# Kernel tuning notes

Measured on AMD Instinct MI355X. Metric: run time of the kernel, lower is better.

## Reference

```python
import jax, jax.numpy as jnp
import numpy as np

B, N, C = 4, 4096, 1024
NUM_HEADS = 16
HEAD_DIM = C // NUM_HEADS


def setup_inputs() -> dict:
    key = jax.random.key(0)
    k1, k2, k3, k4 = jax.random.split(key, 4)
    s_in = 1.0 / np.sqrt(C)
    return {
        "x": jax.random.normal(k1, (B, N, C), dtype=jnp.float32),
        "H": 64,
        "W": 64,
        "Wqkv": jax.random.normal(k2, (3 * C, C), dtype=jnp.float32) * s_in,
        "Wproj": jax.random.normal(k3, (C, C), dtype=jnp.float32) * s_in,
        "bproj": jnp.zeros((C,), dtype=jnp.float32),
        "alpha": jnp.ones((NUM_HEADS,), dtype=jnp.float32),
    }


def reference(x, H, W, Wqkv, Wproj, bproj, alpha):
    Bb, Nn, Cc = x.shape
    h, d = NUM_HEADS, HEAD_DIM
    # qkv: [B, N, 3C] -> [3, B, h, N, d]
    qkv = jnp.einsum('bnc,oc->bno', x, Wqkv)
    qkv = qkv.reshape(Bb, Nn, 3, h, d).transpose(2, 0, 3, 1, 4)
    q, k, v = qkv[0], qkv[1], qkv[2]  # each [B, h, N, d]
    # channel attention: contract over tokens N -> [B, h, d, d]
    attn = jnp.einsum('bhnd,bhne->bhde', k, q) / alpha[None, :, None, None]
    attn = jax.nn.softmax(attn, axis=-1)
    # (dropout is identity in eval/reference mode)
    # head_out: [B, h, d, N] -> transpose -> [B, N, h, d] -> concat heads
    out = jnp.einsum('bhde,bhne->bhdn', attn, v)
    out = out.transpose(0, 3, 1, 2).reshape(Bb, Nn, Cc)
    return jnp.einsum('bnc,oc->bno', out, Wproj) + bproj
```

## Files before the change

### kernel.cpp

```cpp
#include <hip/hip_runtime.h>
#include <hip/hip_bf16.h>
#include <cstdint>
#include <cstddef>

typedef unsigned short u16;
typedef __bf16 bf16x8 __attribute__((ext_vector_type(8)));
typedef float f32x4 __attribute__((ext_vector_type(4)));
typedef unsigned short u16x4 __attribute__((ext_vector_type(4)));
typedef unsigned short u16x8 __attribute__((ext_vector_type(8)));

#define AS1(p) ((__attribute__((address_space(1))) void*)(p))
#define AS3(p) ((__attribute__((address_space(3))) void*)(p))

__device__ __forceinline__ float bf2f(u16 u) {
  unsigned v = ((unsigned)u) << 16; float f; __builtin_memcpy(&f, &v, 4); return f;
}
__device__ __forceinline__ u16 f2bf(float f) {
  unsigned u; __builtin_memcpy(&u, &f, 4);
  u += 0x7FFFu + ((u >> 16) & 1u);
  return (u16)(u >> 16);
}

__global__ __launch_bounds__(256) void convert_kernel(const float* __restrict__ src,
                                                      u16* __restrict__ dst, int n4) {
  int i = blockIdx.x * blockDim.x + threadIdx.x;
  int stride = gridDim.x * blockDim.x;
  for (; i < n4; i += stride) {
    float4 v = ((const float4*)src)[i];
    u16x4 o;
    o.x = f2bf(v.x); o.y = f2bf(v.y); o.z = f2bf(v.z); o.w = f2bf(v.w);
    ((u16x4*)dst)[i] = o;
  }
}

__global__ __launch_bounds__(256) void convert_split_kernel(const float* __restrict__ src,
                                                            u16* __restrict__ hi,
                                                            u16* __restrict__ lo, int n4) {
  int i = blockIdx.x * blockDim.x + threadIdx.x;
  int stride = gridDim.x * blockDim.x;
  for (; i < n4; i += stride) {
    float4 v = ((const float4*)src)[i];
    u16x4 oh, ol;
    oh.x = f2bf(v.x); ol.x = f2bf(v.x - bf2f(oh.x));
    oh.y = f2bf(v.y); ol.y = f2bf(v.y - bf2f(oh.y));
    oh.z = f2bf(v.z); ol.z = f2bf(v.z - bf2f(oh.z));
    oh.w = f2bf(v.w); ol.w = f2bf(v.w - bf2f(oh.w));
    ((u16x4*)hi)[i] = oh;
    ((u16x4*)lo)[i] = ol;
  }
}

__global__ __launch_bounds__(256) void transpose_split_kernel(const float* __restrict__ x,
                                                              u16* __restrict__ Xb,
                                                              u16* __restrict__ XThi,
                                                              u16* __restrict__ XTlo) {
  __shared__ u16 lhi[64 * 72];
  __shared__ u16 llo[64 * 72];
  const int t  = threadIdx.x;
  const int nT = blockIdx.x, cT = blockIdx.y, b = blockIdx.z;
  const size_t xbase = ((size_t)b * 4096 + nT * 64) * 1024 + cT * 64;
  const int c4 = (t & 15) * 4;
  const int r0 = t >> 4;
#pragma unroll
  for (int j = 0; j < 4; ++j) {
    int r = r0 + j * 16;
    float4 v = *(const float4*)(x + xbase + (size_t)r * 1024 + c4);
    u16x4 hi;
    hi.x = f2bf(v.x); hi.y = f2bf(v.y); hi.z = f2bf(v.z); hi.w = f2bf(v.w);
    *(u16x4*)(Xb + xbase + (size_t)r * 1024 + c4) = hi;
    u16 lo[4];
    lo[0] = f2bf(v.x - bf2f(hi.x)); lo[1] = f2bf(v.y - bf2f(hi.y));
    lo[2] = f2bf(v.z - bf2f(hi.z)); lo[3] = f2bf(v.w - bf2f(hi.w));
    u16 hia[4] = { hi.x, hi.y, hi.z, hi.w };
#pragma unroll
    for (int i = 0; i < 4; ++i) {
      lhi[(c4 + i) * 72 + r] = hia[i];
      llo[(c4 + i) * 72 + r] = lo[i];
    }
  }
  __syncthreads();
  const int c  = t >> 2;
  const int n0 = (t & 3) * 16;
  const size_t tbase = ((size_t)b * 1024 + cT * 64 + c) * 4096 + nT * 64 + n0;
  *(u16x8*)(XThi + tbase)     = *(const u16x8*)(lhi + c * 72 + n0);
  *(u16x8*)(XThi + tbase + 8) = *(const u16x8*)(lhi + c * 72 + n0 + 8);
  *(u16x8*)(XTlo + tbase)     = *(const u16x8*)(llo + c * 72 + n0);
  *(u16x8*)(XTlo + tbase + 8) = *(const u16x8*)(llo + c * 72 + n0 + 8);
}

template<bool OUT_BF16, bool HAS_BIAS>
__global__ __launch_bounds__(512, 2) void gemm_pipe(const u16* __restrict__ A,
                                                    const u16* __restrict__ B,
                                                    void* __restrict__ Cv,
                                                    const float* __restrict__ bias,
                                                    int M, int N, int K,
                                                    size_t sA, size_t sB, size_t sC) {
  __shared__ __align__(16) u16 lds[4][2][8192];
  const int tid  = threadIdx.x;
  const int lane = tid & 63;
  const int wave = tid >> 6;
  const int wm = wave >> 2, wn = wave & 3;
  const int rowTile = blockIdx.x * 256;
  const int colTile = blockIdx.y * 256;
  A += (size_t)blockIdx.z * sA;
  B += (size_t)blockIdx.z * sB;

  size_t srcA[2], srcB[2];
  int ldsOff[2];
#pragma unroll
  for (int j = 0; j < 2; ++j) {
    const int L = j * 512 + tid;
    const int sr = L >> 3;
    const int slot = (L & 7) ^ (sr & 7);
    const int r  = (sr << 1) | (slot >> 2);
    const int kq = slot & 3;
    srcA[j] = (size_t)(rowTile + r) * K + kq * 8;
    srcB[j] = (size_t)(colTile + r) * K + kq * 8;
    ldsOff[j] = (j * 512 + (tid & 448)) * 16;
  }

  const int m15 = lane & 15, kq4 = lane >> 4;
  const int r0a = wm * 128 + m15, sa0 = r0a >> 1;
  const int idxA0 = sa0 * 64 + (((((r0a & 1) << 2) | kq4)) ^ (sa0 & 7)) * 8;
  const int r0b = wn * 64 + m15, sb0 = r0b >> 1;
  const int idxB0 = sb0 * 64 + (((((r0b & 1) << 2) | kq4)) ^ (sb0 & 7)) * 8;

  const int NT = K >> 5;

  auto stageA = [&](int tt) {
    char* d = (char*)&lds[tt & 3][0][0];
    const int kt = tt << 5;
#pragma unroll
    for (int j = 0; j < 2; ++j)
      __builtin_amdgcn_global_load_lds(AS1(A + srcA[j] + kt), AS3(d + ldsOff[j]), 16, 0, 0);
  };
  auto stageB = [&](int tt) {
    char* d = (char*)&lds[tt & 3][1][0];
    const int kt = tt << 5;
#pragma unroll
    for (int j = 0; j < 2; ++j)
      __builtin_amdgcn_global_load_lds(AS1(B + srcB[j] + kt), AS3(d + ldsOff[j]), 16, 0, 0);
  };

  stageA(0); stageB(0);
  if (NT > 1) { stageA(1); stageB(1); }
  if (NT > 2) { stageA(2); stageB(2); }
  if (NT > 2) asm volatile("s_waitcnt vmcnt(8)" ::: "memory");
  else        asm volatile("s_waitcnt vmcnt(0)" ::: "memory");
  __builtin_amdgcn_sched_barrier(0);
  __builtin_amdgcn_s_barrier();
  __builtin_amdgcn_sched_barrier(0);

  f32x4 acc[8][4] = {};
  for (int t = 0; t < NT; ++t) {
    const u16* bufA = &lds[t & 3][0][0];
    const u16* bufB = &lds[t & 3][1][0];
    bf16x8 a[8], bfr[4];
#pragma unroll
    for (int ni = 0; ni < 4; ++ni) bfr[ni] = *(const bf16x8*)(bufB + idxB0 + ni * 512);
#pragma unroll
    for (int mi = 0; mi < 4; ++mi) a[mi] = *(const bf16x8*)(bufA + idxA0 + mi * 512);
    if (t + 3 < NT) stageA(t + 3);
    __builtin_amdgcn_sched_barrier(0);
    __builtin_amdgcn_s_barrier();
    __builtin_amdgcn_sched_barrier(0);
    __builtin_amdgcn_s_setprio(1);
#pragma unroll
    for (int mi = 0; mi < 4; ++mi)
#pragma unroll
      for (int ni = 0; ni < 4; ++ni)
        acc[mi][ni] = __builtin_amdgcn_mfma_f32_16x16x32_bf16(a[mi], bfr[ni], acc[mi][ni], 0, 0, 0);
    __builtin_amdgcn_s_setprio(0);
    __builtin_amdgcn_sched_barrier(0);
    __builtin_amdgcn_s_barrier();
    __builtin_amdgcn_sched_barrier(0);
#pragma unroll
    for (int mi = 4; mi < 8; ++mi) a[mi] = *(const bf16x8*)(bufA + idxA0 + mi * 512);
    if (t + 3 < NT) stageB(t + 3);
    __builtin_amdgcn_sched_barrier(0);
    __builtin_amdgcn_s_barrier();
    __builtin_amdgcn_sched_barrier(0);
    __builtin_amdgcn_s_setprio(1);
#pragma unroll
    for (int mi = 4; mi < 8; ++mi)
#pragma unroll
      for (int ni = 0; ni < 4; ++ni)
        acc[mi][ni] = __builtin_amdgcn_mfma_f32_16x16x32_bf16(a[mi], bfr[ni], acc[mi][ni], 0, 0, 0);
    __builtin_amdgcn_s_setprio(0);
    if (t < NT - 1) {
      if (t + 3 < NT)      asm volatile("s_waitcnt vmcnt(8)" ::: "memory");
      else if (t + 2 < NT) asm volatile("s_waitcnt vmcnt(4)" ::: "memory");
      else                 asm volatile("s_waitcnt vmcnt(0)" ::: "memory");
    }
    __builtin_amdgcn_sched_barrier(0);
    __builtin_amdgcn_s_barrier();
    __builtin_amdgcn_sched_barrier(0);
  }

  const int crow0 = rowTile + wm * 128 + (lane >> 4) * 4;
  const int ccol0 = colTile + wn * 64 + m15;
  if constexpr (OUT_BF16) {
    u16* C = (u16*)Cv + (size_t)blockIdx.z * sC;
#pragma unroll
    for (int mi = 0; mi < 8; ++mi)
#pragma unroll
      for (int ni = 0; ni < 4; ++ni) {
        const int col = ccol0 + ni * 16;
        const float bv = HAS_BIAS ? bias[col] : 0.f;
#pragma unroll
        for (int r = 0; r < 4; ++r)
          C[(size_t)(crow0 + mi * 16 + r) * N + col] = f2bf(acc[mi][ni][r] + bv);
      }
  } else {
    float* C = (float*)Cv + (size_t)blockIdx.z * sC;
#pragma unroll
    for (int mi = 0; mi < 8; ++mi)
#pragma unroll
      for (int ni = 0; ni < 4; ++ni) {
        const int col = ccol0 + ni * 16;
        const float bv = HAS_BIAS ? bias[col] : 0.f;
#pragma unroll
        for (int r = 0; r < 4; ++r)
          C[(size_t)(crow0 + mi * 16 + r) * N + col] = acc[mi][ni][r] + bv;
      }
  }
}

__device__ __forceinline__ void pipe4_core(const u16* __restrict__ pAh,
                                           const u16* __restrict__ pAl,
                                           const u16* __restrict__ pBh,
                                           const u16* __restrict__ pBl,
                                           u16* lds, int ldsByteOff,
                                           int idxA0, int idxB0, int NT,
                                           f32x4 acc[4][2]) {
  auto stage2A = [&](int tt) {
    u16* d = lds + (tt & 3) * 16384;
    const int kt = tt << 5;
    __builtin_amdgcn_global_load_lds(AS1(pAh + kt), AS3((char*)d + ldsByteOff), 16, 0, 0);
    __builtin_amdgcn_global_load_lds(AS1(pAl + kt), AS3((char*)(d + 4096) + ldsByteOff), 16, 0, 0);
  };
  auto stage2B = [&](int tt) {
    u16* d = lds + (tt & 3) * 16384 + 8192;
    const int kt = tt << 5;
    __builtin_amdgcn_global_load_lds(AS1(pBh + kt), AS3((char*)d + ldsByteOff), 16, 0, 0);
    __builtin_amdgcn_global_load_lds(AS1(pBl + kt), AS3((char*)(d + 4096) + ldsByteOff), 16, 0, 0);
  };

  stage2A(0); stage2B(0);
  stage2A(1); stage2B(1);
  stage2A(2); stage2B(2);
  asm volatile("s_waitcnt vmcnt(8)" ::: "memory");
  __builtin_amdgcn_sched_barrier(0);
  __builtin_amdgcn_s_barrier();
  __builtin_amdgcn_sched_barrier(0);

  for (int t = 0; t < NT; ++t) {
    const u16* base = lds + (t & 3) * 16384;
    bf16x8 ah[4], al[4], bh[2], bl[2];
    bh[0] = *(const bf16x8*)(base + 8192 + idxB0);
    bh[1] = *(const bf16x8*)(base + 8192 + idxB0 + 512);
    bl[0] = *(const bf16x8*)(base + 12288 + idxB0);
    bl[1] = *(const bf16x8*)(base + 12288 + idxB0 + 512);
    ah[0] = *(const bf16x8*)(base + idxA0);
    ah[1] = *(const bf16x8*)(base + idxA0 + 512);
    al[0] = *(const bf16x8*)(base + 4096 + idxA0);
    al[1] = *(const bf16x8*)(base + 4096 + idxA0 + 512);
    if (t + 3 < NT) stage2A(t + 3);
    __builtin_amdgcn_sched_barrier(0);
    __builtin_amdgcn_s_barrier();
    __builtin_amdgcn_sched_barrier(0);
    __builtin_amdgcn_s_setprio(1);
#pragma unroll
    for (int mi = 0; mi < 2; ++mi)
#pragma unroll
      for (int ni = 0; ni < 2; ++ni) {
        acc[mi][ni] = __builtin_amdgcn_mfma_f32_16x16x32_bf16(ah[mi], bh[ni], acc[mi][ni], 0, 0, 0);
        acc[mi][ni] = __builtin_amdgcn_mfma_f32_16x16x32_bf16(ah[mi], bl[ni], acc[mi][ni], 0, 0, 0);
        acc[mi][ni] = __builtin_amdgcn_mfma_f32_16x16x32_bf16(al[mi], bh[ni], acc[mi][ni], 0, 0, 0);
      }
    __builtin_amdgcn_s_setprio(0);
    __builtin_amdgcn_sched_barrier(0);
    __builtin_amdgcn_s_barrier();
    __builtin_amdgcn_sched_barrier(0);
    ah[2] = *(const bf16x8*)(base + idxA0 + 1024);
    ah[3] = *(const bf16x8*)(base + idxA0 + 1536);
    al[2] = *(const bf16x8*)(base + 4096 + idxA0 + 1024);
    al[3] = *(const bf16x8*)(base + 4096 + idxA0 + 1536);
    if (t + 3 < NT) stage2B(t + 3);
    __builtin_amdgcn_sched_barrier(0);
    __builtin_amdgcn_s_barrier();
    __builtin_amdgcn_sched_barrier(0);
    __builtin_amdgcn_s_setprio(1);
#pragma unroll
    for (int mi = 2; mi < 4; ++mi)
#pragma unroll
      for (int ni = 0; ni < 2; ++ni) {
        acc[mi][ni] = __builtin_amdgcn_mfma_f32_16x16x32_bf16(ah[mi], bh[ni], acc[mi][ni], 0, 0, 0);
        acc[mi][ni] = __builtin_amdgcn_mfma_f32_16x16x32_bf16(ah[mi], bl[ni], acc[mi][ni], 0, 0, 0);
        acc[mi][ni] = __builtin_amdgcn_mfma_f32_16x16x32_bf16(al[mi], bh[ni], acc[mi][ni], 0, 0, 0);
      }
    __builtin_amdgcn_s_setprio(0);
    if (t < NT - 1) {
      if (t + 3 < NT)      asm volatile("s_waitcnt vmcnt(8)" ::: "memory");
      else if (t + 2 < NT) asm volatile("s_waitcnt vmcnt(4)" ::: "memory");
      else                 asm volatile("s_waitcnt vmcnt(0)" ::: "memory");
    }
    __builtin_amdgcn_sched_barrier(0);
    __builtin_amdgcn_s_barrier();
    __builtin_amdgcn_sched_barrier(0);
  }
}

__global__ __launch_bounds__(512, 2) void gram_pipe(const u16* __restrict__ XThi,
                                                    const u16* __restrict__ XTlo,
                                                    float* __restrict__ Gpart) {
  __shared__ __align__(16) u16 lds[4 * 4 * 4096];
  const int tid = threadIdx.x, lane = tid & 63, wave = tid >> 6;
  const int wm = wave >> 2, wn = wave & 3;
  const int bid = blockIdx.x;
  int b, rT, cT, slice, k0, NT;
  if (bid < 64) {
    b = bid & 3; const int j = bid >> 2;
    rT = cT = j >> 1; slice = j & 1; k0 = slice * 2048; NT = 64;
  } else {
    const int e = bid - 64; b = e & 3;
    const int idx = e >> 2; const int tile = idx >> 2, kq = idx & 3;
    int t = tile, rt = 0;
    while (t >= 7 - rt) { t -= 7 - rt; ++rt; }
    const int ct = rt + 1 + t;
    rT = rt; cT = ct;
    if (kq >= 2) { rT = ct; cT = rt; }
    slice = kq & 1; k0 = kq * 1024; NT = 32;
  }
  const int rowTile = rT * 128, colTile = cT * 128;
  const u16* Ah = XThi + ((size_t)b << 22);
  const u16* Al = XTlo + ((size_t)b << 22);

  const int sr = tid >> 3;
  const int slot = (tid & 7) ^ (sr & 7);
  const int r = (sr << 1) | (slot >> 2);
  const int kq8 = (slot & 3) * 8;
  const u16* pAh = Ah + (size_t)(rowTile + r) * 4096 + k0 + kq8;
  const u16* pAl = Al + (size_t)(rowTile + r) * 4096 + k0 + kq8;
  const u16* pBh = Ah + (size_t)(colTile + r) * 4096 + k0 + kq8;
  const u16* pBl = Al + (size_t)(colTile + r) * 4096 + k0 + kq8;
  const int ldsByteOff = (tid & 448) * 16;

  const int m15 = lane & 15, kq4 = lane >> 4;
  const int r0a = wm * 64 + m15, sa0 = r0a >> 1;
  const int idxA0 = sa0 * 64 + (((((r0a & 1) << 2) | kq4)) ^ (sa0 & 7)) * 8;
  const int r0b = wn * 32 + m15, sb0 = r0b >> 1;
  const int idxB0 = sb0 * 64 + (((((r0b & 1) << 2) | kq4)) ^ (sb0 & 7)) * 8;

  f32x4 acc[4][2] = {};
  pipe4_core(pAh, pAl, pBh, pBl, lds, ldsByteOff, idxA0, idxB0, NT, acc);

  float* out = Gpart + ((size_t)(slice * 4 + b) << 20);
  const int crow0 = rowTile + wm * 64 + (lane >> 4) * 4;
  const int ccol0 = colTile + wn * 32 + m15;
#pragma unroll
  for (int mi = 0; mi < 4; ++mi)
#pragma unroll
    for (int ni = 0; ni < 2; ++ni)
#pragma unroll
      for (int r4 = 0; r4 < 4; ++r4)
        out[(size_t)(crow0 + mi * 16 + r4) * 1024 + ccol0 + ni * 16] = acc[mi][ni][r4];
}

__global__ __launch_bounds__(256) void gram_reduce_split(const float* __restrict__ Gp,
                                                         u16* __restrict__ Ghi,
                                                         u16* __restrict__ Glo) {
  const int rt = blockIdx.x, ct = blockIdx.y, b = blockIdx.z;
  const bool diag128 = (rt >> 1) == (ct >> 1);
  const float* s0 = Gp + ((size_t)b << 20);
  const float* s1 = Gp + ((size_t)(4 + b) << 20);
  __shared__ float lT[64 * 68];
  const int t = threadIdx.x;
  const int r = t >> 2;
  const int c16 = (t & 3) * 16;

  if (!diag128) {
    const size_t bb = (size_t)(ct * 64 + r) * 1024 + rt * 64 + c16;
#pragma unroll
    for (int q = 0; q < 4; ++q) {
      float4 v0 = *(const float4*)(s0 + bb + q * 4);
      float4 v1 = *(const float4*)(s1 + bb + q * 4);
      float4 s = { v0.x + v1.x, v0.y + v1.y, v0.z + v1.z, v0.w + v1.w };
      *(float4*)(lT + r * 68 + c16 + q * 4) = s;
    }
    __syncthreads();
  }

  const size_t ab = (size_t)(rt * 64 + r) * 1024 + ct * 64 + c16;
  const size_t ob = ((size_t)b << 20) + ab;
#pragma unroll
  for (int q = 0; q < 4; ++q) {
    float4 v0 = *(const float4*)(s0 + ab + q * 4);
    float4 v1 = *(const float4*)(s1 + ab + q * 4);
    float g[4] = { v0.x + v1.x, v0.y + v1.y, v0.z + v1.z, v0.w + v1.w };
    if (!diag128) {
#pragma unroll
      for (int i = 0; i < 4; ++i) g[i] += lT[(c16 + q * 4 + i) * 68 + r];
    }
    u16x4 oh, ol;
    oh.x = f2bf(g[0]); ol.x = f2bf(g[0] - bf2f(oh.x));
    oh.y = f2bf(g[1]); ol.y = f2bf(g[1] - bf2f(oh.y));
    oh.z = f2bf(g[2]); ol.z = f2bf(g[2] - bf2f(oh.z));
    oh.w = f2bf(g[3]); ol.w = f2bf(g[3] - bf2f(oh.w));
    *(u16x4*)(Ghi + ob + q * 4) = oh;
    *(u16x4*)(Glo + ob + q * 4) = ol;
  }
}

__global__ __launch_bounds__(512, 2) void tprime_pipe(const u16* __restrict__ Wqh,
                                                      const u16* __restrict__ Wql,
                                                      const u16* __restrict__ Ghi,
                                                      const u16* __restrict__ Glo,
                                                      u16* __restrict__ Tph,
                                                      u16* __restrict__ Tpl) {
  __shared__ __align__(16) u16 lds[4 * 4 * 4096];
  const int tid = threadIdx.x, lane = tid & 63, wave = tid >> 6;
  const int wm = wave >> 2, wn = wave & 3;
  const int bid = blockIdx.x;
  const int b = bid & 3, tile = bid >> 2;
  const int rowTile = (tile >> 3) * 128, colTile = (tile & 7) * 128;
  const size_t zoff = (size_t)b << 20;

  const int sr = tid >> 3;
  const int slot = (tid & 7) ^ (sr & 7);
  const int r = (sr << 1) | (slot >> 2);
  const int kq8 = (slot & 3) * 8;
  const u16* pAh = Wqh + (size_t)(rowTile + r) * 1024 + kq8;
  const u16* pAl = Wql + (size_t)(rowTile + r) * 1024 + kq8;
  const u16* pBh = Ghi + zoff + (size_t)(colTile + r) * 1024 + kq8;
  const u16* pBl = Glo + zoff + (size_t)(colTile + r) * 1024 + kq8;
  const int ldsByteOff = (tid & 448) * 16;

  const int m15 = lane & 15, kq4 = lane >> 4;
  const int r0a = wm * 64 + m15, sa0 = r0a >> 1;
  const int idxA0 = sa0 * 64 + (((((r0a & 1) << 2) | kq4)) ^ (sa0 & 7)) * 8;
  const int r0b = wn * 32 + m15, sb0 = r0b >> 1;
  const int idxB0 = sb0 * 64 + (((((r0b & 1) << 2) | kq4)) ^ (sb0 & 7)) * 8;

  f32x4 acc[4][2] = {};
  pipe4_core(pAh, pAl, pBh, pBl, lds, ldsByteOff, idxA0, idxB0, 32, acc);

  const int crow0 = rowTile + wm * 64 + (lane >> 4) * 4;
  const int ccol0 = colTile + wn * 32 + m15;
#pragma unroll
  for (int mi = 0; mi < 4; ++mi)
#pragma unroll
    for (int ni = 0; ni < 2; ++ni)
#pragma unroll
      for (int r4 = 0; r4 < 4; ++r4) {
        float v = acc[mi][ni][r4];
        u16 hi = f2bf(v);
        u16 lo = f2bf(v - bf2f(hi));
        size_t off = zoff + (size_t)(crow0 + mi * 16 + r4) * 1024 + ccol0 + ni * 16;
        Tph[off] = hi;
        Tpl[off] = lo;
      }
}

__global__ __launch_bounds__(256) void s_softmax_kernel(const u16* __restrict__ Wqh,
                                                        const u16* __restrict__ Wql,
                                                        const u16* __restrict__ Tph,
                                                        const u16* __restrict__ Tpl,
                                                        const float* __restrict__ alpha,
                                                        u16* __restrict__ attnT) {
  const int h = blockIdx.x, b = blockIdx.y;
  const int tid = threadIdx.x, lane = tid & 63, wave = tid >> 6;
  __shared__ __align__(16) u16 lAh[64 * 32];
  __shared__ __align__(16) u16 lAl[64 * 32];
  __shared__ __align__(16) u16 lBh[64 * 32];
  __shared__ __align__(16) u16 lBl[64 * 32];

  const size_t aBase = (size_t)(1024 + h * 64) * 1024;
  const size_t bBase = ((size_t)b << 20) + (size_t)(h * 64) * 1024;

  f32x4 acc[4] = {};
  const int m  = lane & 15;
  const int ko = (lane >> 4) * 8;
  const int srow = tid >> 2;
  const int skc  = (tid & 3) * 8;
  const int ldsOff = (tid & 192) * 16;

  for (int kt = 0; kt < 1024; kt += 32) {
    __builtin_amdgcn_global_load_lds(AS1(Wqh + aBase + (size_t)srow * 1024 + kt + skc),
                                     AS3((char*)lAh + ldsOff), 16, 0, 0);
    __builtin_amdgcn_global_load_lds(AS1(Wql + aBase + (size_t)srow * 1024 + kt + skc),
                                     AS3((char*)lAl + ldsOff), 16, 0, 0);
    __builtin_amdgcn_global_load_lds(AS1(Tph + bBase + (size_t)srow * 1024 + kt + skc),
                                     AS3((char*)lBh + ldsOff), 16, 0, 0);
    __builtin_amdgcn_global_load_lds(AS1(Tpl + bBase + (size_t)srow * 1024 + kt + skc),
                                     AS3((char*)lBl + ldsOff), 16, 0, 0);
    __syncthreads();
    bf16x8 ah = *(const bf16x8*)(lAh + (wave * 16 + m) * 32 + ko);
    bf16x8 al = *(const bf16x8*)(lAl + (wave * 16 + m) * 32 + ko);
#pragma unroll
    for (int cb = 0; cb < 4; ++cb) {
      bf16x8 bh = *(const bf16x8*)(lBh + (cb * 16 + m) * 32 + ko);
      bf16x8 bl = *(const bf16x8*)(lBl + (cb * 16 + m) * 32 + ko);
      acc[cb] = __builtin_amdgcn_mfma_f32_16x16x32_bf16(ah, bh, acc[cb], 0, 0, 0);
      acc[cb] = __builtin_amdgcn_mfma_f32_16x16x32_bf16(ah, bl, acc[cb], 0, 0, 0);
      acc[cb] = __builtin_amdgcn_mfma_f32_16x16x32_bf16(al, bh, acc[cb], 0, 0, 0);
    }
    __syncthreads();
  }

  const float invA = 1.f / alpha[h];
  const int g = lane >> 4;
  const size_t obase = (size_t)(b * 16 + h) * 4096;
#pragma unroll
  for (int r = 0; r < 4; ++r) {
    int d = wave * 16 + g * 4 + r;
    float s[4];
#pragma unroll
    for (int cb = 0; cb < 4; ++cb) s[cb] = acc[cb][r] * invA;
    float mx = fmaxf(fmaxf(s[0], s[1]), fmaxf(s[2], s[3]));
#pragma unroll
    for (int o = 1; o < 16; o <<= 1) mx = fmaxf(mx, __shfl_xor(mx, o, 64));
    float e[4]; float sum = 0.f;
#pragma unroll
    for (int cb = 0; cb < 4; ++cb) { e[cb] = __expf(s[cb] - mx); sum += e[cb]; }
#pragma unroll
    for (int o = 1; o < 16; o <<= 1) sum += __shfl_xor(sum, o, 64);
    float inv = 1.f / sum;
#pragma unroll
    for (int cb = 0; cb < 4; ++cb) {
      int e_idx = cb * 16 + (lane & 15);
      attnT[obase + (size_t)e_idx * 64 + d] = f2bf(e[cb] * inv);
    }
  }
}

__global__ __launch_bounds__(256) void m_build_kernel(const u16* __restrict__ Wpb,
                                                      const u16* __restrict__ attnT,
                                                      u16* __restrict__ Mb) {
  const int oT = blockIdx.x, h = blockIdx.y, b = blockIdx.z;
  const int tid = threadIdx.x, lane = tid & 63, wave = tid >> 6;
  __shared__ __align__(16) u16 lA[128 * 64];
  __shared__ __align__(16) u16 lB[64 * 64];
  const int bh = b * 16 + h;
#pragma unroll
  for (int i = 0; i < 4; ++i) {
    int idx = i * 256 + tid;
    int row = idx >> 3;
    int kc  = (idx & 7) * 8;
    int ldsOff = (i * 256 + (tid & 192)) * 16;
    __builtin_amdgcn_global_load_lds(AS1(Wpb + (size_t)(oT * 128 + row) * 1024 + h * 64 + kc),
                                     AS3((char*)lA + ldsOff), 16, 0, 0);
  }
#pragma unroll
  for (int i = 0; i < 2; ++i) {
    int idx = i * 256 + tid;
    int ldsOff = (i * 256 + (tid & 192)) * 16;
    __builtin_amdgcn_global_load_lds(AS1(attnT + (size_t)bh * 4096 + idx * 8),
                                     AS3((char*)lB + ldsOff), 16, 0, 0);
  }
  __syncthreads();
  const int m  = lane & 15;
  const int ko = (lane >> 4) * 8;
  const int wr = wave * 32;
  f32x4 acc[2][4] = {};
#pragma unroll
  for (int ks = 0; ks < 2; ++ks) {
#pragma unroll
    for (int rb = 0; rb < 2; ++rb) {
      bf16x8 a = *(const bf16x8*)(lA + (wr + rb * 16 + m) * 64 + ks * 32 + ko);
#pragma unroll
      for (int cb = 0; cb < 4; ++cb) {
        bf16x8 bb = *(const bf16x8*)(lB + (cb * 16 + m) * 64 + ks * 32 + ko);
        acc[rb][cb] = __builtin_amdgcn_mfma_f32_16x16x32_bf16(a, bb, acc[rb][cb], 0, 0, 0);
      }
    }
  }
  u16* out = Mb + ((size_t)b << 20);
#pragma unroll
  for (int rb = 0; rb < 2; ++rb)
#pragma unroll
    for (int cb = 0; cb < 4; ++cb) {
      int col = h * 64 + cb * 16 + (lane & 15);
#pragma unroll
      for (int r = 0; r < 4; ++r) {
        int row = oT * 128 + wr + rb * 16 + (lane >> 4) * 4 + r;
        out[(size_t)row * 1024 + col] = f2bf(acc[rb][cb][r]);
      }
    }
}

extern "C" void kernel_launch(void* const* d_in, const int* in_sizes, int n_in,
                              void* d_out, int out_size, void* d_ws, size_t ws_size,
                              hipStream_t stream) {
  const float* x     = (const float*)d_in[0];
  const float* Wqkv  = (const float*)d_in[3];
  const float* Wproj = (const float*)d_in[4];
  const float* bproj = (const float*)d_in[5];
  const float* alpha = (const float*)d_in[6];

  char* ws = (char*)d_ws;
  u16*   Xb     = (u16*)ws;
  float* Gpart  = (float*)ws;
  u16*   Mb     = (u16*)ws;
  u16*   XThi   = (u16*)(ws + 33554432);
  u16*   attnTb = (u16*)(ws + 33554432);
  u16*   XTlo  = (u16*)(ws + 67108864);
  u16*   Ghi   = (u16*)(ws + 67108864);
  u16*   Glo   = (u16*)(ws + 75497472);
  u16*   Tph   = (u16*)(ws + 83886080);
  u16*   Tpl   = (u16*)(ws + 92274688);
  u16*   Wqh   = (u16*)(ws + 100663296);
  u16*   Wql   = (u16*)(ws + 106954752);
  u16*   Vb    = (u16*)(ws + 113246208);
  u16*   Wpb   = (u16*)(ws + 146800640);

  transpose_split_kernel<<<dim3(64, 16, 4), 256, 0, stream>>>(x, Xb, XThi, XTlo);
  convert_split_kernel<<<256, 256, 0, stream>>>(Wqkv, Wqh, Wql, 3145728 / 4);
  convert_kernel<<<128, 256, 0, stream>>>(Wproj, Wpb, 1048576 / 4);
  gemm_pipe<true, false><<<dim3(64, 4, 1), 512, 0, stream>>>(
      Xb, Wqh + (size_t)2048 * 1024, Vb, nullptr, 16384, 1024, 1024,
      (size_t)0, (size_t)0, (size_t)0);
  gram_pipe<<<dim3(512), 512, 0, stream>>>(XThi, XTlo, Gpart);
  gram_reduce_split<<<dim3(16, 16, 4), 256, 0, stream>>>(Gpart, Ghi, Glo);
  tprime_pipe<<<dim3(256), 512, 0, stream>>>(Wqh, Wql, Ghi, Glo, Tph, Tpl);
  s_softmax_kernel<<<dim3(16, 4), 256, 0, stream>>>(Wqh, Wql, Tph, Tpl, alpha, attnTb);
  m_build_kernel<<<dim3(8, 16, 4), 256, 0, stream>>>(Wpb, attnTb, Mb);
  gemm_pipe<false, true><<<dim3(16, 4, 4), 512, 0, stream>>>(
      Vb, Mb, (float*)d_out, bproj, 4096, 1024, 1024,
      (size_t)1 << 22, (size_t)1 << 20, (size_t)1 << 22);
}
```

Before: 381.8 us.

## Share A/B tile loads for diagonal Gram tiles, rebalance K-splits, swizzle transpose LDS

The Gram kernel's diagonal blocks, where row and column tiles coincide, now load only the A operand and read B from the same LDS region. This halves their global-to-LDS traffic, and the vmcnt waits are adjusted to match. Off-diagonal blocks switch from equal K quarters to uneven K bands (64/48/8/8 steps), apparently to balance per-block work against the heavier diagonal blocks. The transpose-split kernel XOR-swizzles its LDS row index to reduce bank conflicts, at the cost of more complex indexing and vmcnt bookkeeping that must stay correct.

```diff
diff --git a/kernel.cpp b/kernel.cpp
--- a/kernel.cpp
+++ b/kernel.cpp
@@ -61,6 +61,7 @@
   const size_t xbase = ((size_t)b * 4096 + nT * 64) * 1024 + cT * 64;
   const int c4 = (t & 15) * 4;
   const int r0 = t >> 4;
+  const int rot_w = (t & 3) << 4;
 #pragma unroll
   for (int j = 0; j < 4; ++j) {
     int r = r0 + j * 16;
@@ -72,20 +73,23 @@
     lo[0] = f2bf(v.x - bf2f(hi.x)); lo[1] = f2bf(v.y - bf2f(hi.y));
     lo[2] = f2bf(v.z - bf2f(hi.z)); lo[3] = f2bf(v.w - bf2f(hi.w));
     u16 hia[4] = { hi.x, hi.y, hi.z, hi.w };
+    const int rs = r ^ rot_w;
 #pragma unroll
     for (int i = 0; i < 4; ++i) {
-      lhi[(c4 + i) * 72 + r] = hia[i];
-      llo[(c4 + i) * 72 + r] = lo[i];
+      lhi[(c4 + i) * 72 + rs] = hia[i];
+      llo[(c4 + i) * 72 + rs] = lo[i];
     }
   }
   __syncthreads();
   const int c  = t >> 2;
   const int n0 = (t & 3) * 16;
+  const int rot_r = ((t >> 4) & 3) << 4;
+  const int nA = n0 ^ rot_r;
   const size_t tbase = ((size_t)b * 1024 + cT * 64 + c) * 4096 + nT * 64 + n0;
-  *(u16x8*)(XThi + tbase)     = *(const u16x8*)(lhi + c * 72 + n0);
-  *(u16x8*)(XThi + tbase + 8) = *(const u16x8*)(lhi + c * 72 + n0 + 8);
-  *(u16x8*)(XTlo + tbase)     = *(const u16x8*)(llo + c * 72 + n0);
-  *(u16x8*)(XTlo + tbase + 8) = *(const u16x8*)(llo + c * 72 + n0 + 8);
+  *(u16x8*)(XThi + tbase)     = *(const u16x8*)(lhi + c * 72 + nA);
+  *(u16x8*)(XThi + tbase + 8) = *(const u16x8*)(lhi + c * 72 + nA + 8);
+  *(u16x8*)(XTlo + tbase)     = *(const u16x8*)(llo + c * 72 + nA);
+  *(u16x8*)(XTlo + tbase + 8) = *(const u16x8*)(llo + c * 72 + nA + 8);
 }
 
 template<bool OUT_BF16, bool HAS_BIAS>
@@ -226,12 +230,13 @@
   }
 }
 
+template<int L>
 __device__ __forceinline__ void pipe4_core(const u16* __restrict__ pAh,
                                            const u16* __restrict__ pAl,
                                            const u16* __restrict__ pBh,
                                            const u16* __restrict__ pBl,
                                            u16* lds, int ldsByteOff,
-                                           int idxA0, int idxB0, int NT,
+                                           int idxA0, int idxB0, int bOff, int NT,
                                            f32x4 acc[4][2]) {
   auto stage2A = [&](int tt) {
     u16* d = lds + (tt & 3) * 16384;
@@ -240,16 +245,19 @@
     __builtin_amdgcn_global_load_lds(AS1(pAl + kt), AS3((char*)(d + 4096) + ldsByteOff), 16, 0, 0);
   };
   auto stage2B = [&](int tt) {
-    u16* d = lds + (tt & 3) * 16384 + 8192;
-    const int kt = tt << 5;
-    __builtin_amdgcn_global_load_lds(AS1(pBh + kt), AS3((char*)d + ldsByteOff), 16, 0, 0);
-    __builtin_amdgcn_global_load_lds(AS1(pBl + kt), AS3((char*)(d + 4096) + ldsByteOff), 16, 0, 0);
+    if constexpr (L == 4) {
+      u16* d = lds + (tt & 3) * 16384 + 8192;
+      const int kt = tt << 5;
+      __builtin_amdgcn_global_load_lds(AS1(pBh + kt), AS3((char*)d + ldsByteOff), 16, 0, 0);
+      __builtin_amdgcn_global_load_lds(AS1(pBl + kt), AS3((char*)(d + 4096) + ldsByteOff), 16, 0, 0);
+    }
   };
 
   stage2A(0); stage2B(0);
   stage2A(1); stage2B(1);
   stage2A(2); stage2B(2);
-  asm volatile("s_waitcnt vmcnt(8)" ::: "memory");
+  if constexpr (L == 4) asm volatile("s_waitcnt vmcnt(8)" ::: "memory");
+  else                  asm volatile("s_waitcnt vmcnt(4)" ::: "memory");
   __builtin_amdgcn_sched_barrier(0);
   __builtin_amdgcn_s_barrier();
   __builtin_amdgcn_sched_barrier(0);
@@ -257,10 +265,10 @@
   for (int t = 0; t < NT; ++t) {
     const u16* base = lds + (t & 3) * 16384;
     bf16x8 ah[4], al[4], bh[2], bl[2];
-    bh[0] = *(const bf16x8*)(base + 8192 + idxB0);
-    bh[1] = *(const bf16x8*)(base + 8192 + idxB0 + 512);
-    bl[0] = *(const bf16x8*)(base + 12288 + idxB0);
-    bl[1] = *(const bf16x8*)(base + 12288 + idxB0 + 512);
+    bh[0] = *(const bf16x8*)(base + bOff + idxB0);
+    bh[1] = *(const bf16x8*)(base + bOff + idxB0 + 512);
+    bl[0] = *(const bf16x8*)(base + bOff + 4096 + idxB0);
+    bl[1] = *(const bf16x8*)(base + bOff + 4096 + idxB0 + 512);
     ah[0] = *(const bf16x8*)(base + idxA0);
     ah[1] = *(const bf16x8*)(base + idxA0 + 512);
     al[0] = *(const bf16x8*)(base + 4096 + idxA0);
@@ -301,9 +309,15 @@
       }
     __builtin_amdgcn_s_setprio(0);
     if (t < NT - 1) {
-      if (t + 3 < NT)      asm volatile("s_waitcnt vmcnt(8)" ::: "memory");
-      else if (t + 2 < NT) asm volatile("s_waitcnt vmcnt(4)" ::: "memory");
-      else                 asm volatile("s_waitcnt vmcnt(0)" ::: "memory");
+      if constexpr (L == 4) {
+        if (t + 3 < NT)      asm volatile("s_waitcnt vmcnt(8)" ::: "memory");
+        else if (t + 2 < NT) asm volatile("s_waitcnt vmcnt(4)" ::: "memory");
+        else                 asm volatile("s_waitcnt vmcnt(0)" ::: "memory");
+      } else {
+        if (t + 3 < NT)      asm volatile("s_waitcnt vmcnt(4)" ::: "memory");
+        else if (t + 2 < NT) asm volatile("s_waitcnt vmcnt(2)" ::: "memory");
+        else                 asm volatile("s_waitcnt vmcnt(0)" ::: "memory");
+      }
     }
     __builtin_amdgcn_sched_barrier(0);
     __builtin_amdgcn_s_barrier();
@@ -318,19 +332,22 @@
   const int tid = threadIdx.x, lane = tid & 63, wave = tid >> 6;
   const int wm = wave >> 2, wn = wave & 3;
   const int bid = blockIdx.x;
-  int b, rT, cT, slice, k0, NT;
+  int b, rT, cT, slice, k0, NT; bool same = false;
   if (bid < 64) {
-    b = bid & 3; const int j = bid >> 2;
-    rT = cT = j >> 1; slice = j & 1; k0 = slice * 2048; NT = 64;
+    b = bid & 3; const int j2 = bid >> 2;
+    rT = cT = j2 >> 1; slice = j2 & 1; k0 = slice * 2048; NT = 64; same = true;
   } else {
-    const int e = bid - 64; b = e & 3;
-    const int idx = e >> 2; const int tile = idx >> 2, kq = idx & 3;
-    int t = tile, rt = 0;
+    const int q = bid - 64;
+    const int band = q / 112;
+    const int e = q % 112;
+    b = e & 3; const int pr = e >> 2;
+    int t = pr, rt = 0;
     while (t >= 7 - rt) { t -= 7 - rt; ++rt; }
     const int ct = rt + 1 + t;
-    rT = rt; cT = ct;
-    if (kq >= 2) { rT = ct; cT = rt; }
-    slice = kq & 1; k0 = kq * 1024; NT = 32;
+    constexpr int K0s[4] = {0, 2048, 3584, 3840};
+    constexpr int NTs[4] = {64, 48, 8, 8};
+    k0 = K0s[band]; NT = NTs[band]; slice = band & 1;
+    if (band < 2) { rT = rt; cT = ct; } else { rT = ct; cT = rt; }
   }
   const int rowTile = rT * 128, colTile = cT * 128;
   const u16* Ah = XThi + ((size_t)b << 22);
@@ -353,7 +370,8 @@
   const int idxB0 = sb0 * 64 + (((((r0b & 1) << 2) | kq4)) ^ (sb0 & 7)) * 8;
 
   f32x4 acc[4][2] = {};
-  pipe4_core(pAh, pAl, pBh, pBl, lds, ldsByteOff, idxA0, idxB0, NT, acc);
+  if (same) pipe4_core<2>(pAh, pAl, pAh, pAl, lds, ldsByteOff, idxA0, idxB0, 0, NT, acc);
+  else      pipe4_core<4>(pAh, pAl, pBh, pBl, lds, ldsByteOff, idxA0, idxB0, 8192, NT, acc);
 
   float* out = Gpart + ((size_t)(slice * 4 + b) << 20);
   const int crow0 = rowTile + wm * 64 + (lane >> 4) * 4;
@@ -443,7 +461,7 @@
   const int idxB0 = sb0 * 64 + (((((r0b & 1) << 2) | kq4)) ^ (sb0 & 7)) * 8;
 
   f32x4 acc[4][2] = {};
-  pipe4_core(pAh, pAl, pBh, pBl, lds, ldsByteOff, idxA0, idxB0, 32, acc);
+  pipe4_core<4>(pAh, pAl, pBh, pBl, lds, ldsByteOff, idxA0, idxB0, 8192, 32, acc);
 
   const int crow0 = rowTile + wm * 64 + (lane >> 4) * 4;
   const int ccol0 = colTile + wn * 32 + m15;
```

New measurement: 382.5 us. Within noise of the previous version (+0.2%).
